# Optimization experiments

Measured on AMD Instinct MI355X. Metric: run time of the kernel, lower is better.

The kernel has to match this reference:

```python
import jax, jax.numpy as jnp
import numpy as np

B, N, K = 2, 16384, 16
D_IN, D_OUT = 32, 32
D = 2 * D_OUT      # 64
D8 = D // 8        # 8
EPS = 1e-5
NEG_SLOPE = 0.2


def _bn_params(key, c):
    k1, k2, k3, k4 = jax.random.split(key, 4)
    gamma = 1.0 + 0.1 * jax.random.normal(k1, (c,))
    beta = 0.1 * jax.random.normal(k2, (c,))
    mean = 0.1 * jax.random.normal(k3, (c,))
    var = 0.5 + 0.5 * jax.random.uniform(k4, (c,))
    return jnp.stack([gamma, beta, mean, var])  # (4, c)


def conv1x1(x, W, b=None):
    # x: (B, C, N, K), W: (O, C) -> (B, O, N, K)
    y = jnp.einsum('bcnk,oc->bonk', x, W)
    if b is not None:
        y = y + b[None, :, None, None]
    return y


def bn(x, p):
    # eval-mode BatchNorm2d; p: (4, C) = [gamma, beta, mean, var]
    g, b, m, v = p[0], p[1], p[2], p[3]
    s = g / jnp.sqrt(v + EPS)
    return x * s[None, :, None, None] + (b - m * s)[None, :, None, None]


def lrelu(x):
    return jnp.where(x >= 0, x, NEG_SLOPE * x)


def gather_neighbour(pc, idx):
    # pc: (B, N, D), idx: (B, N, K) -> (B, N, K, D)
    b, n, k = idx.shape
    g = jnp.take_along_axis(pc, idx.reshape(b, n * k, 1), axis=1)
    return g.reshape(b, n, k, pc.shape[-1])


def setup_inputs() -> dict:
    key = jax.random.key(0)
    ks = jax.random.split(key, 24)
    sc = lambda i, shape: jax.random.normal(ks[i], shape) * 0.05
    return {
        'feature': jax.random.normal(ks[0], (B, D_IN, N, 1), dtype=jnp.float32),
        'xyz': jax.random.normal(ks[1], (B, N, 3), dtype=jnp.float32),
        'W1': sc(2, (D, D_IN)), 'bn1': _bn_params(ks[3], D),
        'Wq': sc(4, (D, D)), 'bq': sc(5, (D,)),
        'Wk': sc(6, (D, D)), 'bk': sc(7, (D,)),
        'Wv': sc(8, (D, D)), 'bv': sc(9, (D,)),
        'Wp1': sc(10, (3, 3)), 'bnp1': _bn_params(ks[11], 3),
        'Wp2': sc(12, (D, 3)), 'bp2': sc(13, (D,)),
        'bnw0': _bn_params(ks[14], D),
        'Ww1': sc(15, (D8, D)), 'bnw1': _bn_params(ks[16], D8),
        'Ww2': sc(17, (D8, D8)), 'bw2': sc(18, (D8,)),
        'bn_mid': _bn_params(ks[19], D),
        'W2': sc(20, (D, D)), 'bn2': _bn_params(ks[21], D),
        'neigh_idx': jax.random.randint(ks[22], (B, N, K), 0, N),
    }


def reference(feature, xyz, W1, bn1, Wq, bq, Wk, bk, Wv, bv,
              Wp1, bnp1, Wp2, bp2, bnw0, Ww1, bnw1, Ww2, bw2,
              bn_mid, W2, bn2, neigh_idx):
    # conv1: conv + BN + ReLU
    f = jax.nn.relu(bn(conv1x1(feature, W1), bn1))          # (B, D, N, 1)
    x_q = conv1x1(f, Wq, bq)                                 # (B, D, N, 1)

    k_lin = conv1x1(f, Wk, bk)[:, :, :, 0].transpose(0, 2, 1)  # (B, N, D)
    v_lin = conv1x1(f, Wv, bv)[:, :, :, 0].transpose(0, 2, 1)
    x_k = gather_neighbour(k_lin, neigh_idx).transpose(0, 3, 1, 2)  # (B, D, N, K)
    x_v = gather_neighbour(v_lin, neigh_idx).transpose(0, 3, 1, 2)

    p_g = gather_neighbour(xyz, neigh_idx).transpose(0, 3, 1, 2)    # (B, 3, N, K)
    p_r = conv1x1(jax.nn.relu(bn(conv1x1(p_g, Wp1), bnp1)), Wp2, bp2)  # (B, D, N, K)

    r_qk = x_k - x_q + p_r                                   # broadcast x_q over K

    # linear_w: BN -> LeakyReLU -> conv+BN+ReLU -> conv
    w = lrelu(bn(r_qk, bnw0))
    w = jax.nn.relu(bn(conv1x1(w, Ww1), bnw1))
    w = conv1x1(w, Ww2, bw2)                                 # (B, D8, N, K)
    w = jax.nn.softmax(w, axis=-1)                           # softmax over K

    xp = (x_v + p_r).transpose(0, 2, 3, 1).reshape(B, N, K, 8, D8)
    ws = w.transpose(0, 2, 3, 1)[:, :, :, None, :]           # (B, N, K, 1, D8)
    x = (xp * ws).sum(axis=2).reshape(B, N, D)               # grouped weighted sum over K
    x = x.transpose(0, 2, 1)[..., None]                      # (B, D, N, 1)

    x = lrelu(bn(x, bn_mid))
    x = bn(conv1x1(x, W2), bn2)                              # conv2: conv + BN, no act
    return lrelu(f + x)
```

## Files before the change

kernel.cpp:

```cpp
#include <hip/hip_runtime.h>
#include <hip/hip_bf16.h>
#include <math.h>

#define NPTS 16384
#define KNBR 16
#define EPSV 1e-5f

__device__ __forceinline__ float lrelu_(float x){ return fmaxf(x, 0.2f*x); }
__device__ __forceinline__ float rfl(float x){
    return __uint_as_float((unsigned)__builtin_amdgcn_readfirstlane(__float_as_uint(x)));
}
__device__ __forceinline__ unsigned pk2(float lo, float hi){
    __hip_bfloat16 a = __float2bfloat16(lo), b = __float2bfloat16(hi);
    unsigned short ua = *reinterpret_cast<unsigned short*>(&a);
    unsigned short ub = *reinterpret_cast<unsigned short*>(&b);
    return (unsigned)ua | ((unsigned)ub << 16);
}
__device__ __forceinline__ unsigned short f2bs(float x){
    __hip_bfloat16 a = __float2bfloat16(x);
    return *reinterpret_cast<unsigned short*>(&a);
}
__device__ __forceinline__ void unpk(unsigned u, float& lo, float& hi){
    lo = __uint_as_float(u << 16);
    hi = __uint_as_float(u & 0xffff0000u);
}

__global__ __launch_bounds__(256,3) void qkvf_kernel(
    const float* __restrict__ feature,
    const float* __restrict__ W1, const float* __restrict__ bn1,
    const float* __restrict__ Wq, const float* __restrict__ bq,
    const float* __restrict__ Wk, const float* __restrict__ bk,
    const float* __restrict__ Wv, const float* __restrict__ bv,
    float* __restrict__ f_ws, float* __restrict__ q_ws,
    unsigned short* __restrict__ kv_ws)
{
    __shared__ unsigned lw1h[64*20];
    __shared__ unsigned lwqh[64*36];
    __shared__ unsigned lwkh[64*36];
    __shared__ unsigned lwvh[64*36];
    __shared__ float lbq[64], lbk[64], lbv[64], ls1[64], lt1[64];

    const int t = threadIdx.x;
#pragma unroll
    for (int r=0;r<4;++r){
        const int idx = t + r*256;
        const int o = idx>>4, c2 = idx&15;
        lw1h[o*20+c2] = pk2(W1[o*32+2*c2], W1[o*32+2*c2+1]);
    }
#pragma unroll
    for (int r=0;r<8;++r){
        const int idx = t + r*256;
        const int o = idx>>5, c2 = idx&31;
        lwqh[o*36+c2] = pk2(Wq[o*64+2*c2], Wq[o*64+2*c2+1]);
        lwkh[o*36+c2] = pk2(Wk[o*64+2*c2], Wk[o*64+2*c2+1]);
        lwvh[o*36+c2] = pk2(Wv[o*64+2*c2], Wv[o*64+2*c2+1]);
    }
    if (t<64){
        lbq[t]=bq[t]; lbk[t]=bk[t]; lbv[t]=bv[t];
        const float s = bn1[t]*rsqrtf(bn1[192+t]+EPSV);
        ls1[t]=s; lt1[t]=fmaf(-bn1[128+t], s, bn1[64+t]);
    }
    __syncthreads();

    const int tid   = blockIdx.x*256 + t;
    const int ll    = t & 7;
    const int p     = tid >> 3;
    const int b     = p >> 14;
    const int n     = p & (NPTS-1);
    const int obase = (t & 63) & 56;

    float ft[4];
    const float* fbase = feature + b*32*NPTS + n;
#pragma unroll
    for (int u=0;u<4;++u) ft[u] = fbase[(8*u+ll)*NPTS];

    float Yf0[4],Yf1[4],Yf2[4],Yf3[4],Yf4[4],Yf5[4],Yf6[4],Yf7[4];
#pragma unroll
    for (int u=0;u<4;++u){
        Yf0[u]=__shfl(ft[u], obase+0); Yf1[u]=__shfl(ft[u], obase+1);
        Yf2[u]=__shfl(ft[u], obase+2); Yf3[u]=__shfl(ft[u], obase+3);
        Yf4[u]=__shfl(ft[u], obase+4); Yf5[u]=__shfl(ft[u], obase+5);
        Yf6[u]=__shfl(ft[u], obase+6); Yf7[u]=__shfl(ft[u], obase+7);
    }

    float fv[8];
#pragma unroll
    for (int i=0;i<8;++i){
        const int o = 8*i+ll;
        const uint4* row = (const uint4*)(lw1h + o*20);
        float hs = 0.f;
#pragma unroll
        for (int g=0;g<4;++g){
            const uint4 w = row[g];
            float a,c;
            unpk(w.x,a,c); hs=fmaf(a,Yf0[g],hs); hs=fmaf(c,Yf1[g],hs);
            unpk(w.y,a,c); hs=fmaf(a,Yf2[g],hs); hs=fmaf(c,Yf3[g],hs);
            unpk(w.z,a,c); hs=fmaf(a,Yf4[g],hs); hs=fmaf(c,Yf5[g],hs);
            unpk(w.w,a,c); hs=fmaf(a,Yf6[g],hs); hs=fmaf(c,Yf7[g],hs);
        }
        fv[i] = fmaxf(fmaf(hs, ls1[o], lt1[o]), 0.f);
        f_ws[p*64+o] = fv[i];
    }

    float Y0[8],Y1[8],Y2[8],Y3[8],Y4[8],Y5[8],Y6[8],Y7[8];
#pragma unroll
    for (int u=0;u<8;++u){
        Y0[u]=__shfl(fv[u], obase+0); Y1[u]=__shfl(fv[u], obase+1);
        Y2[u]=__shfl(fv[u], obase+2); Y3[u]=__shfl(fv[u], obase+3);
        Y4[u]=__shfl(fv[u], obase+4); Y5[u]=__shfl(fv[u], obase+5);
        Y6[u]=__shfl(fv[u], obase+6); Y7[u]=__shfl(fv[u], obase+7);
    }

#define QKV_ROWS(LWH, LBIAS, STORE_STMT)                              \
    _Pragma("unroll")                                                 \
    for (int i=0;i<8;++i){                                            \
        const int o = 8*i+ll;                                         \
        const uint4* row = (const uint4*)(LWH + o*36);                \
        float hs = LBIAS[o];                                          \
        _Pragma("unroll")                                             \
        for (int g=0;g<8;++g){                                        \
            const uint4 w = row[g];                                   \
            float a,c;                                                \
            unpk(w.x,a,c); hs=fmaf(a,Y0[g],hs); hs=fmaf(c,Y1[g],hs);  \
            unpk(w.y,a,c); hs=fmaf(a,Y2[g],hs); hs=fmaf(c,Y3[g],hs);  \
            unpk(w.z,a,c); hs=fmaf(a,Y4[g],hs); hs=fmaf(c,Y5[g],hs);  \
            unpk(w.w,a,c); hs=fmaf(a,Y6[g],hs); hs=fmaf(c,Y7[g],hs);  \
        }                                                             \
        STORE_STMT;                                                   \
    }

    QKV_ROWS(lwqh, lbq, q_ws[p*64+o] = hs)
    QKV_ROWS(lwkh, lbk, kv_ws[p*128+o] = f2bs(hs))
    QKV_ROWS(lwvh, lbv, kv_ws[p*128+64+o] = f2bs(hs))
#undef QKV_ROWS
}

__global__ __launch_bounds__(256) void attn_kernel(
    const float* __restrict__ xyz, const int* __restrict__ nidx,
    const float* __restrict__ Wp1, const float* __restrict__ bnp1,
    const float* __restrict__ Wp2, const float* __restrict__ bp2,
    const float* __restrict__ bnw0,
    const float* __restrict__ Ww1, const float* __restrict__ bnw1,
    const float* __restrict__ Ww2, const float* __restrict__ bw2,
    const float* __restrict__ bn_mid,
    const float* __restrict__ W2, const float* __restrict__ bn2,
    const float* __restrict__ f_ws, const float* __restrict__ q_ws,
    const unsigned short* __restrict__ kv_ws,
    float* __restrict__ out)
{
    __shared__ unsigned lww1h[8*32];
    __shared__ float lw2[64*68];
    __shared__ float lout[64*33];
    const int t = threadIdx.x;
    if (t < 256){
        const int j = t>>5, c2 = t&31;
        lww1h[j*32+c2] = pk2(Ww1[j*64+2*c2], Ww1[j*64+2*c2+1]);
    }
#pragma unroll
    for (int r=0;r<16;++r){
        const int idx = t + r*256;
        const int o = idx>>6, c = idx&63;
        lw2[o*68+c] = W2[idx];
    }
    __syncthreads();

    const int tid = blockIdx.x*256 + t;
    const int ll  = t & 7;
    const int p   = tid >> 3;
    const int b   = p >> 14;
    const int obase = (t & 63) & 56;

    float wp1[9];
#pragma unroll
    for (int u=0;u<9;++u) wp1[u] = rfl(Wp1[u]);
    float sp1[3], tp1[3];
#pragma unroll
    for (int o=0;o<3;++o){
        const float s = bnp1[o]*rsqrtf(bnp1[9+o]+EPSV);
        sp1[o]=rfl(s); tp1[o]=rfl(fmaf(-bnp1[6+o], s, bnp1[3+o]));
    }
    float sw1[8], tw1[8];
#pragma unroll
    for (int j=0;j<8;++j){
        const float s = bnw1[j]*rsqrtf(bnw1[24+j]+EPSV);
        sw1[j]=rfl(s); tw1[j]=rfl(fmaf(-bnw1[16+j], s, bnw1[8+j]));
    }
    float wp2f[24];
#pragma unroll
    for (int u=0;u<6;++u){
        const float4 w = ((const float4*)Wp2)[6*ll+u];
        wp2f[4*u]=w.x; wp2f[4*u+1]=w.y; wp2f[4*u+2]=w.z; wp2f[4*u+3]=w.w;
    }
    float ww2r[8]; float bwr;
    {
        const float4 a = ((const float4*)Ww2)[2*ll], c = ((const float4*)Ww2)[2*ll+1];
        ww2r[0]=a.x; ww2r[1]=a.y; ww2r[2]=a.z; ww2r[3]=a.w;
        ww2r[4]=c.x; ww2r[5]=c.y; ww2r[6]=c.z; ww2r[7]=c.w;
        bwr = bw2[ll];
    }
    float s0[8], qc[8];
    {
        float qv[8], bpv[8];
        const float4* qp = (const float4*)(q_ws + p*64 + 8*ll);
        const float4 q0 = qp[0], q1 = qp[1];
        qv[0]=q0.x;qv[1]=q0.y;qv[2]=q0.z;qv[3]=q0.w; qv[4]=q1.x;qv[5]=q1.y;qv[6]=q1.z;qv[7]=q1.w;
        const float4* bp = (const float4*)(bp2 + 8*ll);
        const float4 b0 = bp[0], b1 = bp[1];
        bpv[0]=b0.x;bpv[1]=b0.y;bpv[2]=b0.z;bpv[3]=b0.w; bpv[4]=b1.x;bpv[5]=b1.y;bpv[6]=b1.z;bpv[7]=b1.w;
        const float4* g4 = (const float4*)(bnw0 + 8*ll);
        const float4 g0=g4[0], g1=g4[1];
        const float4* be4 = (const float4*)(bnw0 + 64 + 8*ll);
        const float4 e0=be4[0], e1=be4[1];
        const float4* m4 = (const float4*)(bnw0 + 128 + 8*ll);
        const float4 m0=m4[0], m1=m4[1];
        const float4* v4 = (const float4*)(bnw0 + 192 + 8*ll);
        const float4 v0=v4[0], v1=v4[1];
        const float gg[8]={g0.x,g0.y,g0.z,g0.w,g1.x,g1.y,g1.z,g1.w};
        const float bb[8]={e0.x,e0.y,e0.z,e0.w,e1.x,e1.y,e1.z,e1.w};
        const float mm[8]={m0.x,m0.y,m0.z,m0.w,m1.x,m1.y,m1.z,m1.w};
        const float vv[8]={v0.x,v0.y,v0.z,v0.w,v1.x,v1.y,v1.z,v1.w};
#pragma unroll
        for (int i=0;i<8;++i){
            const float s = gg[i]*rsqrtf(vv[i]+EPSV);
            s0[i]=s;
            qc[i]=fmaf(-mm[i], s, bb[i]) + s*(bpv[i]-qv[i]);
        }
    }

    float m[8], l[8], acc[8];
#pragma unroll
    for (int j=0;j<8;++j){ m[j]=-3.0e38f; l[j]=0.f; acc[j]=0.f; }

    const int* nip = nidx + p*16;

#pragma unroll 2
    for (int k=0;k<KNBR;++k){
        const int ni   = nip[k];
        const int rowb = (b<<14) + ni;
        const uint4* kvp = (const uint4*)(kv_ws + (size_t)rowb*128);
        const uint4 ku = kvp[ll];
        const uint4 vu = kvp[8+ll];
        const float* xp = xyz + rowb*3;
        const float x0=xp[0], x1=xp[1], x2v=xp[2];

        float t3[3];
#pragma unroll
        for (int o=0;o<3;++o){
            const float u = fmaf(wp1[3*o], x0, fmaf(wp1[3*o+1], x1, wp1[3*o+2]*x2v));
            t3[o] = fmaxf(fmaf(u, sp1[o], tp1[o]), 0.f);
        }
        float kf[8];
        unpk(ku.x, kf[0], kf[1]); unpk(ku.y, kf[2], kf[3]);
        unpk(ku.z, kf[4], kf[5]); unpk(ku.w, kf[6], kf[7]);
        float pr[8], wl[8];
#pragma unroll
        for (int i=0;i<8;++i){
            pr[i] = fmaf(wp2f[3*i], t3[0], fmaf(wp2f[3*i+1], t3[1], wp2f[3*i+2]*t3[2]));
            wl[i] = lrelu_(fmaf(s0[i], kf[i]+pr[i], qc[i]));
        }
        float y[8];
#pragma unroll
        for (int j=0;j<8;++j){
            const uint4 w = *(const uint4*)(lww1h + j*32 + 4*ll);
            float a,c, yy;
            unpk(w.x,a,c); yy  = a*wl[0];        yy = fmaf(c,wl[1],yy);
            unpk(w.y,a,c); yy = fmaf(a,wl[2],yy); yy = fmaf(c,wl[3],yy);
            unpk(w.z,a,c); yy = fmaf(a,wl[4],yy); yy = fmaf(c,wl[5],yy);
            unpk(w.w,a,c); yy = fmaf(a,wl[6],yy); yy = fmaf(c,wl[7],yy);
            yy += __shfl_xor(yy, 1);
            yy += __shfl_xor(yy, 2);
            yy += __shfl_xor(yy, 4);
            y[j] = yy;
        }
#pragma unroll
        for (int j=0;j<8;++j) y[j] = fmaxf(fmaf(y[j], sw1[j], tw1[j]), 0.f);
        float w2own = bwr;
#pragma unroll
        for (int j=0;j<8;++j) w2own = fmaf(ww2r[j], y[j], w2own);
        float w2[8];
        w2[0]=__shfl(w2own, obase+0); w2[1]=__shfl(w2own, obase+1);
        w2[2]=__shfl(w2own, obase+2); w2[3]=__shfl(w2own, obase+3);
        w2[4]=__shfl(w2own, obase+4); w2[5]=__shfl(w2own, obase+5);
        w2[6]=__shfl(w2own, obase+6); w2[7]=__shfl(w2own, obase+7);

        float sc[8], e[8];
#pragma unroll
        for (int j=0;j<8;++j){
            const float mn = fmaxf(m[j], w2[j]);
            sc[j] = __expf(m[j]-mn);
            e[j]  = __expf(w2[j]-mn);
            l[j]  = fmaf(l[j], sc[j], e[j]);
            m[j]  = mn;
        }
        float vf[8];
        unpk(vu.x, vf[0], vf[1]); unpk(vu.y, vf[2], vf[3]);
        unpk(vu.z, vf[4], vf[5]); unpk(vu.w, vf[6], vf[7]);
#pragma unroll
        for (int i=0;i<8;++i)
            acc[i] = fmaf(acc[i], sc[i], (vf[i]+pr[i])*e[i]);
    }

    float xm[8];
    {
        const float4* bp = (const float4*)(bp2 + 8*ll);
        const float4 b0 = bp[0], b1 = bp[1];
        const float bpv[8]={b0.x,b0.y,b0.z,b0.w,b1.x,b1.y,b1.z,b1.w};
        const float4* g4 = (const float4*)(bn_mid + 8*ll);
        const float4 g0=g4[0], g1=g4[1];
        const float4* be4 = (const float4*)(bn_mid + 64 + 8*ll);
        const float4 e0=be4[0], e1=be4[1];
        const float4* m4 = (const float4*)(bn_mid + 128 + 8*ll);
        const float4 m0=m4[0], m1=m4[1];
        const float4* v4 = (const float4*)(bn_mid + 192 + 8*ll);
        const float4 v0=v4[0], v1=v4[1];
        const float gg[8]={g0.x,g0.y,g0.z,g0.w,g1.x,g1.y,g1.z,g1.w};
        const float bb[8]={e0.x,e0.y,e0.z,e0.w,e1.x,e1.y,e1.z,e1.w};
        const float mm[8]={m0.x,m0.y,m0.z,m0.w,m1.x,m1.y,m1.z,m1.w};
        const float vv[8]={v0.x,v0.y,v0.z,v0.w,v1.x,v1.y,v1.z,v1.w};
#pragma unroll
        for (int i=0;i<8;++i){
            const float s = gg[i]*rsqrtf(vv[i]+EPSV);
            const float tt = fmaf(-mm[i], s, bb[i]);
            const float xx = fmaf(acc[i], 1.f/l[i], bpv[i]);
            xm[i] = lrelu_(fmaf(xx, s, tt));
        }
    }
    float Zx0[4],Zx1[4],Zx2[4],Zx3[4],Zx4[4],Zx5[4],Zx6[4],Zx7[4];
    float Zx8[4],Zx9[4],Zx10[4],Zx11[4],Zx12[4],Zx13[4],Zx14[4],Zx15[4];
#pragma unroll
    for (int r=0;r<4;++r){
        Zx0[r] =__shfl(xm[r],   obase+0); Zx1[r] =__shfl(xm[4+r], obase+0);
        Zx2[r] =__shfl(xm[r],   obase+1); Zx3[r] =__shfl(xm[4+r], obase+1);
        Zx4[r] =__shfl(xm[r],   obase+2); Zx5[r] =__shfl(xm[4+r], obase+2);
        Zx6[r] =__shfl(xm[r],   obase+3); Zx7[r] =__shfl(xm[4+r], obase+3);
        Zx8[r] =__shfl(xm[r],   obase+4); Zx9[r] =__shfl(xm[4+r], obase+4);
        Zx10[r]=__shfl(xm[r],   obase+5); Zx11[r]=__shfl(xm[4+r], obase+5);
        Zx12[r]=__shfl(xm[r],   obase+6); Zx13[r]=__shfl(xm[4+r], obase+6);
        Zx14[r]=__shfl(xm[r],   obase+7); Zx15[r]=__shfl(xm[4+r], obase+7);
    }
#define DOT4(W4, Z) (fmaf((W4).w, (Z)[3], fmaf((W4).z, (Z)[2], fmaf((W4).y, (Z)[1], (W4).x*(Z)[0]))))
    const float* fpw = f_ws + p*64;
    const int pidx = t >> 3;
#pragma unroll
    for (int i=0;i<8;++i){
        const int o = 8*i+ll;
        const float4* row = (const float4*)(lw2 + o*68);
        float hs = 0.f;
        hs += DOT4(row[0],  Zx0);  hs += DOT4(row[1],  Zx1);
        hs += DOT4(row[2],  Zx2);  hs += DOT4(row[3],  Zx3);
        hs += DOT4(row[4],  Zx4);  hs += DOT4(row[5],  Zx5);
        hs += DOT4(row[6],  Zx6);  hs += DOT4(row[7],  Zx7);
        hs += DOT4(row[8],  Zx8);  hs += DOT4(row[9],  Zx9);
        hs += DOT4(row[10], Zx10); hs += DOT4(row[11], Zx11);
        hs += DOT4(row[12], Zx12); hs += DOT4(row[13], Zx13);
        hs += DOT4(row[14], Zx14); hs += DOT4(row[15], Zx15);
        const float s2 = bn2[o]*rsqrtf(bn2[192+o]+EPSV);
        const float t2 = fmaf(-bn2[128+o], s2, bn2[64+o]);
        const float x2r = fmaf(hs, s2, t2);
        lout[o*33 + pidx] = lrelu_(fpw[o] + x2r);
    }
#undef DOT4
    __syncthreads();
    {
        const int oc = t >> 2;
        const int j0 = (t & 3) * 8;
        const int p0 = blockIdx.x * 32;
        const int bb = p0 >> 14;
        const int n0 = p0 & (NPTS-1);
        float v0[4], v1[4];
#pragma unroll
        for (int r=0;r<4;++r){ v0[r] = lout[oc*33 + j0 + r]; v1[r] = lout[oc*33 + j0 + 4 + r]; }
        float* op = out + (size_t)(bb*64 + oc)*NPTS + n0 + j0;
        ((float4*)op)[0] = make_float4(v0[0],v0[1],v0[2],v0[3]);
        ((float4*)op)[1] = make_float4(v1[0],v1[1],v1[2],v1[3]);
    }
}

extern "C" void kernel_launch(void* const* d_in, const int* in_sizes, int n_in,
                              void* d_out, int out_size, void* d_ws, size_t ws_size,
                              hipStream_t stream) {
    const float* feature = (const float*)d_in[0];
    const float* xyz     = (const float*)d_in[1];
    const float* W1      = (const float*)d_in[2];
    const float* bn1     = (const float*)d_in[3];
    const float* Wq      = (const float*)d_in[4];
    const float* bq      = (const float*)d_in[5];
    const float* Wk      = (const float*)d_in[6];
    const float* bk      = (const float*)d_in[7];
    const float* Wv      = (const float*)d_in[8];
    const float* bv      = (const float*)d_in[9];
    const float* Wp1     = (const float*)d_in[10];
    const float* bnp1    = (const float*)d_in[11];
    const float* Wp2     = (const float*)d_in[12];
    const float* bp2     = (const float*)d_in[13];
    const float* bnw0    = (const float*)d_in[14];
    const float* Ww1     = (const float*)d_in[15];
    const float* bnw1    = (const float*)d_in[16];
    const float* Ww2     = (const float*)d_in[17];
    const float* bw2     = (const float*)d_in[18];
    const float* bn_mid  = (const float*)d_in[19];
    const float* W2      = (const float*)d_in[20];
    const float* bn2     = (const float*)d_in[21];
    const int*   nidx    = (const int*)d_in[22];
    float* out = (float*)d_out;

    float* ws   = (float*)d_ws;
    float* f_ws = ws;
    float* q_ws = ws + 2097152;
    unsigned short* kv_ws = (unsigned short*)(ws + 4194304);

    qkvf_kernel<<<1024, 256, 0, stream>>>(feature, W1, bn1, Wq, bq, Wk, bk, Wv, bv,
                                          f_ws, q_ws, kv_ws);
    attn_kernel<<<1024, 256, 0, stream>>>(xyz, nidx, Wp1, bnp1, Wp2, bp2, bnw0,
                                          Ww1, bnw1, Ww2, bw2, bn_mid, W2, bn2,
                                          f_ws, q_ws, kv_ws, out);
}
```

Before: 183.6 us.

## Compute f/q/k/v projections with bf16 MFMA and store f and q as bf16

The qkvf kernel is rewritten so the W1, Wq, Wk and Wv projections run on 16x16x32 bf16 MFMA instructions instead of scalar FMAs with shuffles. Features are staged through LDS in bf16, and outputs are assembled in LDS and written out with coalesced uint4 stores. Each block now covers 64 points, so the grid is halved. f and q are also stored as packed bf16 instead of fp32, which halves their workspace traffic into the attention kernel but lowers precision of the residual and query terms.

After: 167.6 us. 1.1x faster.

```diff
diff --git a/kernel.cpp b/kernel.cpp
--- a/kernel.cpp
+++ b/kernel.cpp
@@ -5,6 +5,9 @@
 #define NPTS 16384
 #define KNBR 16
 #define EPSV 1e-5f
+
+typedef __attribute__((ext_vector_type(8))) short bf16x8;
+typedef __attribute__((ext_vector_type(4))) float f32x4;
 
 __device__ __forceinline__ float lrelu_(float x){ return fmaxf(x, 0.2f*x); }
 __device__ __forceinline__ float rfl(float x){
@@ -24,115 +27,129 @@
     lo = __uint_as_float(u << 16);
     hi = __uint_as_float(u & 0xffff0000u);
 }
-
-__global__ __launch_bounds__(256,3) void qkvf_kernel(
+__device__ __forceinline__ bf16x8 mk8(float4 x, float4 y){
+    union { unsigned u[4]; bf16x8 v; } z;
+    z.u[0]=pk2(x.x,x.y); z.u[1]=pk2(x.z,x.w); z.u[2]=pk2(y.x,y.y); z.u[3]=pk2(y.z,y.w);
+    return z.v;
+}
+
+__global__ __launch_bounds__(256) void qkvf_kernel(
     const float* __restrict__ feature,
     const float* __restrict__ W1, const float* __restrict__ bn1,
     const float* __restrict__ Wq, const float* __restrict__ bq,
     const float* __restrict__ Wk, const float* __restrict__ bk,
     const float* __restrict__ Wv, const float* __restrict__ bv,
-    float* __restrict__ f_ws, float* __restrict__ q_ws,
-    unsigned short* __restrict__ kv_ws)
+    unsigned* __restrict__ f_pk, unsigned* __restrict__ q_pk,
+    unsigned* __restrict__ kv_u)
 {
-    __shared__ unsigned lw1h[64*20];
-    __shared__ unsigned lwqh[64*36];
-    __shared__ unsigned lwkh[64*36];
-    __shared__ unsigned lwvh[64*36];
-    __shared__ float lbq[64], lbk[64], lbv[64], ls1[64], lt1[64];
-
-    const int t = threadIdx.x;
+    __shared__ unsigned short lfeat[64*40];
+    __shared__ unsigned lf[64*36];
+    __shared__ unsigned lbuf[64*100];
+
+    const int t    = threadIdx.x;
+    const int lane = t & 63;
+    const int w    = t >> 6;
+    const int i16  = lane & 15;
+    const int g    = lane >> 4;
+    const int p0   = blockIdx.x * 64;
+    const int b    = p0 >> 14;
+    const int n0   = p0 & (NPTS-1);
+
+    {
+        const float* fb = feature + b*32*NPTS + n0;
+#pragma unroll
+        for (int r=0;r<8;++r){
+            const int idx = t + r*256;
+            const int ch = idx >> 6, pt = idx & 63;
+            lfeat[pt*40 + ch] = f2bs(fb[ch*NPTS + pt]);
+        }
+    }
+
+    const int row = 16*w + i16;
+    bf16x8 a1, aq0, aq1, ak0, ak1, av0, av1;
+    {
+        const float4* v4;
+        v4 = (const float4*)(W1 + row*32 + 8*g);  a1  = mk8(v4[0], v4[1]);
+        v4 = (const float4*)(Wq + row*64 + 8*g);  aq0 = mk8(v4[0], v4[1]);
+        v4 = (const float4*)(Wq + row*64 + 32 + 8*g); aq1 = mk8(v4[0], v4[1]);
+        v4 = (const float4*)(Wk + row*64 + 8*g);  ak0 = mk8(v4[0], v4[1]);
+        v4 = (const float4*)(Wk + row*64 + 32 + 8*g); ak1 = mk8(v4[0], v4[1]);
+        v4 = (const float4*)(Wv + row*64 + 8*g);  av0 = mk8(v4[0], v4[1]);
+        v4 = (const float4*)(Wv + row*64 + 32 + 8*g); av1 = mk8(v4[0], v4[1]);
+    }
+    float s1v[4], t1v[4], bqv[4], bkv[4], bvv[4];
 #pragma unroll
     for (int r=0;r<4;++r){
-        const int idx = t + r*256;
-        const int o = idx>>4, c2 = idx&15;
-        lw1h[o*20+c2] = pk2(W1[o*32+2*c2], W1[o*32+2*c2+1]);
-    }
-#pragma unroll
-    for (int r=0;r<8;++r){
-        const int idx = t + r*256;
-        const int o = idx>>5, c2 = idx&31;
-        lwqh[o*36+c2] = pk2(Wq[o*64+2*c2], Wq[o*64+2*c2+1]);
-        lwkh[o*36+c2] = pk2(Wk[o*64+2*c2], Wk[o*64+2*c2+1]);
-        lwvh[o*36+c2] = pk2(Wv[o*64+2*c2], Wv[o*64+2*c2+1]);
-    }
-    if (t<64){
-        lbq[t]=bq[t]; lbk[t]=bk[t]; lbv[t]=bv[t];
-        const float s = bn1[t]*rsqrtf(bn1[192+t]+EPSV);
-        ls1[t]=s; lt1[t]=fmaf(-bn1[128+t], s, bn1[64+t]);
+        const int o = 16*w + 4*g + r;
+        const float s = bn1[o]*rsqrtf(bn1[192+o]+EPSV);
+        s1v[r]=s; t1v[r]=fmaf(-bn1[128+o], s, bn1[64+o]);
+        bqv[r]=bq[o]; bkv[r]=bk[o]; bvv[r]=bv[o];
     }
     __syncthreads();
 
-    const int tid   = blockIdx.x*256 + t;
-    const int ll    = t & 7;
-    const int p     = tid >> 3;
-    const int b     = p >> 14;
-    const int n     = p & (NPTS-1);
-    const int obase = (t & 63) & 56;
-
-    float ft[4];
-    const float* fbase = feature + b*32*NPTS + n;
-#pragma unroll
-    for (int u=0;u<4;++u) ft[u] = fbase[(8*u+ll)*NPTS];
-
-    float Yf0[4],Yf1[4],Yf2[4],Yf3[4],Yf4[4],Yf5[4],Yf6[4],Yf7[4];
-#pragma unroll
-    for (int u=0;u<4;++u){
-        Yf0[u]=__shfl(ft[u], obase+0); Yf1[u]=__shfl(ft[u], obase+1);
-        Yf2[u]=__shfl(ft[u], obase+2); Yf3[u]=__shfl(ft[u], obase+3);
-        Yf4[u]=__shfl(ft[u], obase+4); Yf5[u]=__shfl(ft[u], obase+5);
-        Yf6[u]=__shfl(ft[u], obase+6); Yf7[u]=__shfl(ft[u], obase+7);
-    }
-
-    float fv[8];
-#pragma unroll
-    for (int i=0;i<8;++i){
-        const int o = 8*i+ll;
-        const uint4* row = (const uint4*)(lw1h + o*20);
-        float hs = 0.f;
-#pragma unroll
-        for (int g=0;g<4;++g){
-            const uint4 w = row[g];
-            float a,c;
-            unpk(w.x,a,c); hs=fmaf(a,Yf0[g],hs); hs=fmaf(c,Yf1[g],hs);
-            unpk(w.y,a,c); hs=fmaf(a,Yf2[g],hs); hs=fmaf(c,Yf3[g],hs);
-            unpk(w.z,a,c); hs=fmaf(a,Yf4[g],hs); hs=fmaf(c,Yf5[g],hs);
-            unpk(w.w,a,c); hs=fmaf(a,Yf6[g],hs); hs=fmaf(c,Yf7[g],hs);
-        }
-        fv[i] = fmaxf(fmaf(hs, ls1[o], lt1[o]), 0.f);
-        f_ws[p*64+o] = fv[i];
-    }
-
-    float Y0[8],Y1[8],Y2[8],Y3[8],Y4[8],Y5[8],Y6[8],Y7[8];
-#pragma unroll
-    for (int u=0;u<8;++u){
-        Y0[u]=__shfl(fv[u], obase+0); Y1[u]=__shfl(fv[u], obase+1);
-        Y2[u]=__shfl(fv[u], obase+2); Y3[u]=__shfl(fv[u], obase+3);
-        Y4[u]=__shfl(fv[u], obase+4); Y5[u]=__shfl(fv[u], obase+5);
-        Y6[u]=__shfl(fv[u], obase+6); Y7[u]=__shfl(fv[u], obase+7);
-    }
-
-#define QKV_ROWS(LWH, LBIAS, STORE_STMT)                              \
-    _Pragma("unroll")                                                 \
-    for (int i=0;i<8;++i){                                            \
-        const int o = 8*i+ll;                                         \
-        const uint4* row = (const uint4*)(LWH + o*36);                \
-        float hs = LBIAS[o];                                          \
-        _Pragma("unroll")                                             \
-        for (int g=0;g<8;++g){                                        \
-            const uint4 w = row[g];                                   \
-            float a,c;                                                \
-            unpk(w.x,a,c); hs=fmaf(a,Y0[g],hs); hs=fmaf(c,Y1[g],hs);  \
-            unpk(w.y,a,c); hs=fmaf(a,Y2[g],hs); hs=fmaf(c,Y3[g],hs);  \
-            unpk(w.z,a,c); hs=fmaf(a,Y4[g],hs); hs=fmaf(c,Y5[g],hs);  \
-            unpk(w.w,a,c); hs=fmaf(a,Y6[g],hs); hs=fmaf(c,Y7[g],hs);  \
-        }                                                             \
-        STORE_STMT;                                                   \
-    }
-
-    QKV_ROWS(lwqh, lbq, q_ws[p*64+o] = hs)
-    QKV_ROWS(lwkh, lbk, kv_ws[p*128+o] = f2bs(hs))
-    QKV_ROWS(lwvh, lbv, kv_ws[p*128+64+o] = f2bs(hs))
-#undef QKV_ROWS
+#pragma unroll
+    for (int st=0; st<4; ++st){
+        const int pt = st*16 + i16;
+        bf16x8 b1 = *(const bf16x8*)((const unsigned short*)lfeat + pt*40 + 8*g);
+        f32x4 d = {0.f,0.f,0.f,0.f};
+        d = __builtin_amdgcn_mfma_f32_16x16x32_bf16(a1, b1, d, 0,0,0);
+        const float f0 = fmaxf(fmaf(d[0], s1v[0], t1v[0]), 0.f);
+        const float f1 = fmaxf(fmaf(d[1], s1v[1], t1v[1]), 0.f);
+        const float f2 = fmaxf(fmaf(d[2], s1v[2], t1v[2]), 0.f);
+        const float f3 = fmaxf(fmaf(d[3], s1v[3], t1v[3]), 0.f);
+        const int oh = 8*w + 2*g;
+        lf[pt*36 + oh    ] = pk2(f0, f1);
+        lf[pt*36 + oh + 1] = pk2(f2, f3);
+    }
+    __syncthreads();
+
+#pragma unroll
+    for (int st=0; st<4; ++st){
+        const int pt = st*16 + i16;
+        bf16x8 b20 = *(const bf16x8*)(lf + pt*36 + 4*g);
+        bf16x8 b21 = *(const bf16x8*)(lf + pt*36 + 16 + 4*g);
+        f32x4 dq = {bqv[0],bqv[1],bqv[2],bqv[3]};
+        f32x4 dk = {bkv[0],bkv[1],bkv[2],bkv[3]};
+        f32x4 dv = {bvv[0],bvv[1],bvv[2],bvv[3]};
+        dq = __builtin_amdgcn_mfma_f32_16x16x32_bf16(aq0, b20, dq, 0,0,0);
+        dq = __builtin_amdgcn_mfma_f32_16x16x32_bf16(aq1, b21, dq, 0,0,0);
+        dk = __builtin_amdgcn_mfma_f32_16x16x32_bf16(ak0, b20, dk, 0,0,0);
+        dk = __builtin_amdgcn_mfma_f32_16x16x32_bf16(ak1, b21, dk, 0,0,0);
+        dv = __builtin_amdgcn_mfma_f32_16x16x32_bf16(av0, b20, dv, 0,0,0);
+        dv = __builtin_amdgcn_mfma_f32_16x16x32_bf16(av1, b21, dv, 0,0,0);
+        const int pbase = pt*100;
+        const int oh = 8*w + 2*g;
+        lbuf[pbase + oh         ] = pk2(dq[0], dq[1]);
+        lbuf[pbase + oh + 1     ] = pk2(dq[2], dq[3]);
+        lbuf[pbase + 32 + oh    ] = pk2(dk[0], dk[1]);
+        lbuf[pbase + 32 + oh + 1] = pk2(dk[2], dk[3]);
+        lbuf[pbase + 64 + oh    ] = pk2(dv[0], dv[1]);
+        lbuf[pbase + 64 + oh + 1] = pk2(dv[2], dv[3]);
+    }
+    __syncthreads();
+
+    if (w == 0){
+#pragma unroll
+        for (int c=0;c<8;++c){
+            const int off = c*256 + 4*lane;
+            const int pt = off>>5, j = off&31;
+            *(uint4*)(f_pk + (size_t)p0*32 + off) = *(const uint4*)(lf + pt*36 + j);
+        }
+    } else if (w == 1){
+#pragma unroll
+        for (int c=0;c<8;++c){
+            const int off = c*256 + 4*lane;
+            const int pt = off>>5, j = off&31;
+            *(uint4*)(q_pk + (size_t)p0*32 + off) = *(const uint4*)(lbuf + pt*100 + j);
+        }
+    } else {
+#pragma unroll
+        for (int c=0;c<8;++c){
+            const int off = (w-2)*2048 + c*256 + 4*lane;
+            const int pt = off>>6, j = off&63;
+            *(uint4*)(kv_u + (size_t)p0*64 + off) = *(const uint4*)(lbuf + pt*100 + 32 + j);
+        }
+    }
 }
 
 __global__ __launch_bounds__(256) void attn_kernel(
@@ -144,7 +161,7 @@
     const float* __restrict__ Ww2, const float* __restrict__ bw2,
     const float* __restrict__ bn_mid,
     const float* __restrict__ W2, const float* __restrict__ bn2,
-    const float* __restrict__ f_ws, const float* __restrict__ q_ws,
+    const unsigned* __restrict__ f_pk, const unsigned* __restrict__ q_pk,
     const unsigned short* __restrict__ kv_ws,
     float* __restrict__ out)
 {
@@ -201,9 +218,9 @@
     float s0[8], qc[8];
     {
         float qv[8], bpv[8];
-        const float4* qp = (const float4*)(q_ws + p*64 + 8*ll);
-        const float4 q0 = qp[0], q1 = qp[1];
-        qv[0]=q0.x;qv[1]=q0.y;qv[2]=q0.z;qv[3]=q0.w; qv[4]=q1.x;qv[5]=q1.y;qv[6]=q1.z;qv[7]=q1.w;
+        const uint4 qu = *(const uint4*)(q_pk + (size_t)p*32 + 4*ll);
+        unpk(qu.x, qv[0], qv[1]); unpk(qu.y, qv[2], qv[3]);
+        unpk(qu.z, qv[4], qv[5]); unpk(qu.w, qv[6], qv[7]);
         const float4* bp = (const float4*)(bp2 + 8*ll);
         const float4 b0 = bp[0], b1 = bp[1];
         bpv[0]=b0.x;bpv[1]=b0.y;bpv[2]=b0.z;bpv[3]=b0.w; bpv[4]=b1.x;bpv[5]=b1.y;bpv[6]=b1.z;bpv[7]=b1.w;
@@ -339,7 +356,6 @@
         Zx14[r]=__shfl(xm[r],   obase+7); Zx15[r]=__shfl(xm[4+r], obase+7);
     }
 #define DOT4(W4, Z) (fmaf((W4).w, (Z)[3], fmaf((W4).z, (Z)[2], fmaf((W4).y, (Z)[1], (W4).x*(Z)[0]))))
-    const float* fpw = f_ws + p*64;
     const int pidx = t >> 3;
 #pragma unroll
     for (int i=0;i<8;++i){
@@ -357,7 +373,10 @@
         const float s2 = bn2[o]*rsqrtf(bn2[192+o]+EPSV);
         const float t2 = fmaf(-bn2[128+o], s2, bn2[64+o]);
         const float x2r = fmaf(hs, s2, t2);
-        lout[o*33 + pidx] = lrelu_(fpw[o] + x2r);
+        const unsigned fu = f_pk[(size_t)p*32 + 4*i + (ll>>1)];
+        float flo, fhi; unpk(fu, flo, fhi);
+        const float fo = (ll & 1) ? fhi : flo;
+        lout[o*33 + pidx] = lrelu_(fo + x2r);
     }
 #undef DOT4
     __syncthreads();
@@ -404,14 +423,15 @@
     const int*   nidx    = (const int*)d_in[22];
     float* out = (float*)d_out;
 
-    float* ws   = (float*)d_ws;
-    float* f_ws = ws;
-    float* q_ws = ws + 2097152;
-    unsigned short* kv_ws = (unsigned short*)(ws + 4194304);
-
-    qkvf_kernel<<<1024, 256, 0, stream>>>(feature, W1, bn1, Wq, bq, Wk, bk, Wv, bv,
-                                          f_ws, q_ws, kv_ws);
+    unsigned* ws = (unsigned*)d_ws;
+    unsigned* f_pk = ws;
+    unsigned* q_pk = ws + 1048576;
+    unsigned* kv_u = ws + 2097152;
+    unsigned short* kv_ws = (unsigned short*)kv_u;
+
+    qkvf_kernel<<<512, 256, 0, stream>>>(feature, W1, bn1, Wq, bq, Wk, bk, Wv, bv,
+                                         f_pk, q_pk, kv_u);
     attn_kernel<<<1024, 256, 0, stream>>>(xyz, nidx, Wp1, bnp1, Wp2, bp2, bnw0,
                                           Ww1, bnw1, Ww2, bw2, bn_mid, W2, bn2,
-                                          f_ws, q_ws, kv_ws, out);
-}
+                                          f_pk, q_pk, kv_ws, out);
+}
```
